# Optimization experiments

Hardware: AMD Instinct MI355X
Metric: run time of the kernel (lower is better)

The kernel has to match this reference:

```python
import jax, jax.numpy as jnp
import numpy as np

N_HEADS = 16
NEG_BIG = float(-2**32 + 1)  # value the original writes into masked positions


def setup_inputs() -> dict:
    key = jax.random.key(0)
    ks = jax.random.split(key, 5)
    B, T, D = 64, 256, 1024
    s = 1.0 / np.sqrt(D)
    return {
        "x": jax.random.normal(ks[0], (B, T, D), jnp.float32),
        "pos_emb": jax.random.normal(ks[1], (T, D), jnp.float32),
        "Wq": jax.random.normal(ks[2], (D, D), jnp.float32) * s,
        "Wk": jax.random.normal(ks[3], (D, D), jnp.float32) * s,
        "Wv": jax.random.normal(ks[4], (D, D), jnp.float32) * s,
    }


def reference(x, pos_emb, Wq, Wk, Wv):
    B, T, D = x.shape
    H = N_HEADS
    dh = D // H
    # add position embeddings (same arange positions for every batch row)
    temporal = x + pos_emb[None, :T, :]            # [B, T, D]
    q = temporal @ Wq                              # [B, T, D]
    k = temporal @ Wk
    v = temporal @ Wv
    # chunk along feature dim into H heads, concatenate along batch dim -> [H*B, T, dh]
    def split_heads(t):
        return jnp.concatenate(jnp.split(t, H, axis=2), axis=0)
    q_, k_, v_ = split_heads(q), split_heads(k), split_heads(v)
    scores = jnp.einsum('btd,bsd->bts', q_, k_) / jnp.sqrt(jnp.asarray(T, x.dtype))  # [H*B, T, T]
    # original masks the LOWER triangle (tril > 0 -> padding), faithful to source
    tril = jnp.tril(jnp.ones((T, T), x.dtype))
    scores = jnp.where(tril > 0, jnp.asarray(NEG_BIG, x.dtype), scores)
    # original applies softmax over dim=0 (the batch*head axis), faithful to source
    probs = jax.nn.softmax(scores, axis=0)         # [H*B, T, T]
    out = jnp.einsum('bts,bsd->btd', probs, v_)    # [H*B, T, dh]
    # merge heads back: chunk along batch dim, concatenate along feature dim
    out = jnp.concatenate(jnp.split(out, H, axis=0), axis=-1)  # [B, T, D]
    return out
```

## Files before the change

### kernel.cpp

```cpp
#include <hip/hip_runtime.h>

constexpr int SEQ = 256;
constexpr int DIM = 1024;
constexpr float SCALE = 0.0625f;

typedef __attribute__((ext_vector_type(8))) short bf16x8;
typedef __attribute__((ext_vector_type(4))) float f32x4;
typedef unsigned short ushort_t;
typedef unsigned int uint_t;

__device__ __forceinline__ void gld_lds16(const void* g, void* l) {
  __builtin_amdgcn_global_load_lds(
      (const __attribute__((address_space(1))) unsigned int*)g,
      (__attribute__((address_space(3))) unsigned int*)l, 16, 0, 0);
}

__device__ __forceinline__ ushort_t f2bf(float f) {
  uint_t u = __float_as_uint(f);
  return (ushort_t)((u + 0x7fffu + ((u >> 16) & 1u)) >> 16);
}

__global__ __launch_bounds__(256)
void prep_a(const float* __restrict__ x, const float* __restrict__ pos,
            ushort_t* __restrict__ Ab) {
  const size_t idx = ((size_t)blockIdx.x * 256 + threadIdx.x) * 8;
  const int m = (int)(idx >> 10), k = (int)(idx & 1023);
  float4 x0 = *(const float4*)(x + idx);
  float4 x1 = *(const float4*)(x + idx + 4);
  const float* pp = pos + ((size_t)(m & 255) << 10) + k;
  float4 p0 = *(const float4*)pp;
  float4 p1 = *(const float4*)(pp + 4);
  uint_t w0 = (uint_t)f2bf(x0.x + p0.x) | ((uint_t)f2bf(x0.y + p0.y) << 16);
  uint_t w1 = (uint_t)f2bf(x0.z + p0.z) | ((uint_t)f2bf(x0.w + p0.w) << 16);
  uint_t w2 = (uint_t)f2bf(x1.x + p1.x) | ((uint_t)f2bf(x1.y + p1.y) << 16);
  uint_t w3 = (uint_t)f2bf(x1.z + p1.z) | ((uint_t)f2bf(x1.w + p1.w) << 16);
  *(uint4*)&Ab[idx] = make_uint4(w0, w1, w2, w3);
}

__global__ __launch_bounds__(256)
void pack_w(const float* __restrict__ Wq, const float* __restrict__ Wk,
            const float* __restrict__ Wv, ushort_t* __restrict__ Bp) {
  const float* W = (blockIdx.z == 0) ? Wq : (blockIdx.z == 1) ? Wk : Wv;
  const int n  = blockIdx.x * 256 + threadIdx.x;
  const int k8 = blockIdx.y * 8;
  uint_t h[8];
#pragma unroll
  for (int i = 0; i < 8; ++i) h[i] = f2bf(W[(size_t)(k8 + i) * DIM + n]);
  uint_t hp[4];
#pragma unroll
  for (int j = 0; j < 4; ++j) hp[j] = h[2 * j] | (h[2 * j + 1] << 16);
  const int np = blockIdx.z * 1024 + n;
  const int nb = np >> 8, nl = np & 255;
  const int kc = k8 >> 6, kk = k8 & 63;
  size_t base = (((size_t)nb * 16 + kc) * 256 + nl) * 64 + kk;
  *(uint4*)&Bp[base] = make_uint4(hp[0], hp[1], hp[2], hp[3]);
}

__global__ __launch_bounds__(512, 2)
void qkv_mfma(const ushort_t* __restrict__ Ab, const ushort_t* __restrict__ Bp,
              ushort_t* __restrict__ q_bf, ushort_t* __restrict__ k_bf,
              ushort_t* __restrict__ vT_bf) {
  const int nb = blockIdx.x;
  const int mb = blockIdx.y;
  const int tid = (int)threadIdx.x;
  const int wave = tid >> 6, lane = tid & 63;
  const int wm = wave >> 2, wn = wave & 3;
  const int l15 = lane & 15, quad = lane >> 4;

  __shared__ ushort_t smem[65536];

  const int r8 = lane >> 3;
  const int lc8 = ((lane & 7) ^ r8) * 8;
  const size_t a_row = ((size_t)(mb * 256 + wave * 8 + r8)) << 10;
  const size_t b_row = ((size_t)((nb * 16) * 256 + wave * 8 + r8)) << 6;
  const int wb = wave * 512;

#define SA(q, tt, c) gld_lds16(Ab + a_row + ((size_t)(q) << 16) + (size_t)(tt) * 64 + lc8, \
                               smem + (c) * 32768 + (q) * 4096 + wb)
#define SB(q, tt, c) gld_lds16(Bp + b_row + (size_t)(tt) * 16384 + (q) * 4096 + lc8, \
                               smem + (c) * 32768 + 16384 + (q) * 4096 + wb)

  const int swz = l15 & 7;
  const int cko0 = (quad ^ swz) * 8;
  const int cko1 = ((4 + quad) ^ swz) * 8;
  const int arow0 = (wm * 128 + l15) * 64;
  const int brow0 = (wn * 64 + l15) * 64;

  f32x4 acc[8][4] = {};
  bf16x8 af[4][2], bf[4][2];

#define LDA_II(IH, ii) do { \
    const int ro = arow0 + ((IH) * 64 + (ii) * 16) * 64; \
    af[ii][0] = *(const bf16x8*)&Ac[ro + cko0]; \
    af[ii][1] = *(const bf16x8*)&Ac[ro + cko1]; } while (0)
#define LDB_J(J) do { const int ro = brow0 + (J) * 1024; \
    bf[J][0] = *(const bf16x8*)&Bc[ro + cko0]; \
    bf[J][1] = *(const bf16x8*)&Bc[ro + cko1]; } while (0)
#define MMQ(IH, II0, II1, J0) do { \
    _Pragma("unroll") for (int ks = 0; ks < 2; ++ks) \
    _Pragma("unroll") for (int ii = (II0); ii < (II1); ++ii) \
    _Pragma("unroll") for (int jj = 0; jj < 2; ++jj) \
      acc[(IH) * 4 + ii][(J0) + jj] = __builtin_amdgcn_mfma_f32_16x16x32_bf16( \
          af[ii][ks], bf[(J0) + jj][ks], acc[(IH) * 4 + ii][(J0) + jj], 0, 0, 0); \
    } while (0)

  SA(0, 0, 0); SA(2, 0, 0); SB(0, 0, 0); SB(1, 0, 0); SB(2, 0, 0); SB(3, 0, 0);
  SA(1, 0, 0); SA(3, 0, 0);
  SB(0, 1, 1); SB(1, 1, 1); SA(0, 1, 1); SA(2, 1, 1);
  asm volatile("s_waitcnt vmcnt(6)" ::: "memory");
  __builtin_amdgcn_s_barrier();

  for (int t = 0; t < 16; ++t) {
    const int cur = t & 1, nxt = cur ^ 1;
    const int tn  = (t < 15) ? t + 1 : 15;
    const int tn2 = (t < 14) ? t + 2 : 15;
    const ushort_t* Ac = &smem[cur * 32768];
    const ushort_t* Bc = Ac + 16384;
    LDA_II(0, 0); LDA_II(0, 1); LDA_II(0, 2); LDA_II(0, 3);
    LDB_J(0); LDB_J(1);
    SB(2, tn, nxt); SB(3, tn, nxt);
    __builtin_amdgcn_s_barrier();
    LDB_J(2); LDB_J(3);
    SA(1, tn, nxt); SA(3, tn, nxt);
    asm volatile("s_waitcnt lgkmcnt(4)" ::: "memory");
    __builtin_amdgcn_s_setprio(1);
    MMQ(0, 0, 4, 0);
    __builtin_amdgcn_s_setprio(0);
    asm volatile("s_waitcnt vmcnt(8)" ::: "memory");
    __builtin_amdgcn_s_barrier();
    asm volatile("s_waitcnt lgkmcnt(0)" ::: "memory");
    __builtin_amdgcn_s_setprio(1);
    MMQ(0, 0, 2, 2);
    __builtin_amdgcn_s_setprio(0);
    LDA_II(1, 0); LDA_II(1, 1);
    __builtin_amdgcn_s_setprio(1);
    MMQ(0, 2, 4, 2);
    __builtin_amdgcn_s_setprio(0);
    LDA_II(1, 2); LDA_II(1, 3);
    __builtin_amdgcn_s_barrier();
    SB(0, tn2, cur); SB(1, tn2, cur);
    asm volatile("s_waitcnt lgkmcnt(0)" ::: "memory");
    __builtin_amdgcn_s_setprio(1);
    MMQ(1, 0, 4, 2);
    __builtin_amdgcn_s_setprio(0);
    __builtin_amdgcn_s_barrier();
    SA(0, tn2, cur); SA(2, tn2, cur);
    __builtin_amdgcn_s_setprio(1);
    MMQ(1, 0, 4, 0);
    __builtin_amdgcn_s_setprio(0);
    asm volatile("s_waitcnt vmcnt(6)" ::: "memory");
    __builtin_amdgcn_s_barrier();
  }

  asm volatile("s_waitcnt vmcnt(0)" ::: "memory");
  const int wq = nb >> 2;
  const int h  = (nb & 3) * 4 + wn;
  if (wq < 2) {
    ushort_t* base = ((wq == 0) ? q_bf : k_bf) + (size_t)(mb * 16 + h) * (SEQ * 64);
    const int tb = wm * 128 + quad * 4;
#pragma unroll
    for (int i = 0; i < 8; ++i)
#pragma unroll
      for (int j = 0; j < 4; ++j) {
        const int d = j * 16 + l15;
#pragma unroll
        for (int r = 0; r < 4; ++r)
          base[(size_t)(tb + i * 16 + r) * 64 + d] = f2bf(acc[i][j][r]);
      }
  } else {
    __builtin_amdgcn_s_barrier();
    ushort_t* L = &smem[wave * 4608];
    ushort_t* vbase = vT_bf + (size_t)(mb * 16 + h) * (64 * SEQ) + wm * 128;
    const int tc = (lane & 7) * 8;
#pragma unroll
    for (int g = 0; g < 2; ++g) {
#pragma unroll
      for (int ii = 0; ii < 4; ++ii)
#pragma unroll
        for (int j = 0; j < 4; ++j) {
          f32x4 v = acc[g * 4 + ii][j];
          uint_t lo = (uint_t)f2bf(v[0]) | ((uint_t)f2bf(v[1]) << 16);
          uint_t hi = (uint_t)f2bf(v[2]) | ((uint_t)f2bf(v[3]) << 16);
          *(uint2*)&L[(j * 16 + l15) * 72 + ii * 16 + quad * 4] = make_uint2(lo, hi);
        }
#pragma unroll
      for (int u = 0; u < 8; ++u) {
        const int d = u * 8 + r8;
        uint4 val = *(const uint4*)&L[d * 72 + tc];
        *(uint4*)&vbase[(size_t)d * SEQ + g * 64 + tc] = val;
      }
    }
  }
#undef SA
#undef SB
#undef LDA_II
#undef LDB_J
#undef MMQ
}

__global__ __launch_bounds__(256)
void stats_mfma(const ushort_t* __restrict__ qb, const ushort_t* __restrict__ kb,
                float* __restrict__ part_l) {
  const int p = blockIdx.x, g = blockIdx.y;
  int tt, ss;
  if (p < 4) { tt = p; ss = p; }
  else {
    const int idx = p - 4;
    tt = (idx < 3) ? 0 : (idx < 5) ? 1 : 2;
    ss = (idx < 3) ? idx + 1 : (idx < 5) ? idx - 1 : 3;
  }
  const bool diag = (p < 4);
  const int tid = threadIdx.x, wave = tid >> 6, lane = tid & 63;
  const int l15 = lane & 15, quad = lane >> 4;

  __shared__ __attribute__((aligned(16))) float red[4][64 * 68];

  f32x4 lacc[4][4] = {};

  for (int i4 = 0; i4 < 4; ++i4) {
    const int bp = g * 16 + wave * 4 + i4;
    const int bh = (bp & 63) * 16 + (bp >> 6);
    const ushort_t* qt = qb + (size_t)bh * (SEQ * 64) + (size_t)(tt * 64) * 64;
    const ushort_t* kt = kb + (size_t)bh * (SEQ * 64) + (size_t)(ss * 64) * 64;
    bf16x8 aq[4][2], bk[4][2];
#pragma unroll
    for (int m = 0; m < 4; ++m)
#pragma unroll
      for (int ks = 0; ks < 2; ++ks) {
        aq[m][ks] = *(const bf16x8*)&qt[(m * 16 + l15) * 64 + ks * 32 + quad * 8];
        bk[m][ks] = *(const bf16x8*)&kt[(m * 16 + l15) * 64 + ks * 32 + quad * 8];
      }
    f32x4 sf[4][4] = {};
#pragma unroll
    for (int ks = 0; ks < 2; ++ks)
#pragma unroll
      for (int m = 0; m < 4; ++m)
#pragma unroll
        for (int n = 0; n < 4; ++n)
          sf[m][n] = __builtin_amdgcn_mfma_f32_16x16x32_bf16(aq[m][ks], bk[n][ks], sf[m][n], 0, 0, 0);
#pragma unroll
    for (int m = 0; m < 4; ++m)
#pragma unroll
      for (int n = 0; n < 4; ++n)
#pragma unroll
        for (int r = 0; r < 4; ++r) {
          float e = __expf(sf[m][n][r] * SCALE);
          if (diag) {
            const int t = tt * 64 + m * 16 + quad * 4 + r;
            const int s = ss * 64 + n * 16 + l15;
            e = (s > t) ? e : 1.0f;
          }
          lacc[m][n][r] += e;
        }
  }
  float* R = red[wave];
#pragma unroll
  for (int m = 0; m < 4; ++m)
#pragma unroll
    for (int r = 0; r < 4; ++r) {
      const int row = m * 16 + quad * 4 + r;
#pragma unroll
      for (int n = 0; n < 4; ++n)
        R[row * 68 + n * 16 + l15] = lacc[m][n][r];
    }
  __syncthreads();
  const int trow = tid >> 2, c0 = (tid & 3) * 16;
  const float* r0 = &red[0][trow * 68 + c0];
  const float* r1 = &red[1][trow * 68 + c0];
  const float* r2 = &red[2][trow * 68 + c0];
  const float* r3 = &red[3][trow * 68 + c0];
  float* pl = part_l + (size_t)g * (SEQ * SEQ) + (size_t)(tt * 64 + trow) * SEQ + ss * 64 + c0;
#pragma unroll
  for (int c = 0; c < 16; c += 4) {
    float4 s0 = *(const float4*)&r0[c];
    float4 s1 = *(const float4*)&r1[c];
    float4 s2 = *(const float4*)&r2[c];
    float4 s3 = *(const float4*)&r3[c];
    float4 o;
    o.x = (s0.x + s1.x) + (s2.x + s3.x);
    o.y = (s0.y + s1.y) + (s2.y + s3.y);
    o.z = (s0.z + s1.z) + (s2.z + s3.z);
    o.w = (s0.w + s1.w) + (s2.w + s3.w);
    *(float4*)&pl[c] = o;
  }
}

__global__ __launch_bounds__(256)
void merge_kernel(const float* __restrict__ part_l, float* __restrict__ inv_lT) {
  const int i = blockIdx.x * 256 + threadIdx.x;
  const int t = i >> 8, s = i & 255;
  float invv;
  if (s <= t) invv = 1.0f / 1024.0f;
  else {
    const float* p = part_l + i;
    float a0 = 0.f, a1 = 0.f, a2 = 0.f, a3 = 0.f,
          a4 = 0.f, a5 = 0.f, a6 = 0.f, a7 = 0.f;
    for (int g = 0; g < 64; g += 8) {
      const float* q = p + ((size_t)g << 16);
      a0 += q[0ull << 16]; a1 += q[1ull << 16]; a2 += q[2ull << 16]; a3 += q[3ull << 16];
      a4 += q[4ull << 16]; a5 += q[5ull << 16]; a6 += q[6ull << 16]; a7 += q[7ull << 16];
    }
    invv = 1.0f / (((a0 + a1) + (a2 + a3)) + ((a4 + a5) + (a6 + a7)));
  }
  inv_lT[s * SEQ + t] = invv;
}

__global__ __launch_bounds__(256)
void pv_mfma(const ushort_t* __restrict__ qb, const ushort_t* __restrict__ kb,
             const ushort_t* __restrict__ vtb, const float* __restrict__ inv_lT,
             float* __restrict__ out) {
  const int bh = blockIdx.x;
  const int b = bh >> 4, h = bh & 15;
  const int tid = threadIdx.x, wave = tid >> 6, lane = tid & 63;
  const int l15 = lane & 15, quad = lane >> 4;
  const int t0 = wave * 64;

  __shared__ ushort_t Plds[4][64][72];
  ushort_t (*Pw)[72] = Plds[wave];

  const ushort_t* qq = qb + (size_t)bh * (SEQ * 64);
  const ushort_t* kk = kb + (size_t)bh * (SEQ * 64);
  const ushort_t* vv = vtb + (size_t)bh * (64 * SEQ);

  bf16x8 qf[4][2];
#pragma unroll
  for (int nt = 0; nt < 4; ++nt)
#pragma unroll
    for (int ks = 0; ks < 2; ++ks)
      qf[nt][ks] = *(const bf16x8*)&qq[(t0 + nt * 16 + l15) * 64 + ks * 32 + quad * 8];

  f32x4 o[4][4] = {};

  for (int sc = 0; sc < 4; ++sc) {
    if (sc < wave) {
      const uint_t c = 0x3A803A80u;
      const uint4 cc = make_uint4(c, c, c, c);
#pragma unroll
      for (int u = 0; u < 8; ++u) *(uint4*)&Pw[lane][u * 8] = cc;
    } else {
      bf16x8 kf[4][2];
#pragma unroll
      for (int ms = 0; ms < 4; ++ms)
#pragma unroll
        for (int ks = 0; ks < 2; ++ks)
          kf[ms][ks] = *(const bf16x8*)&kk[(sc * 64 + ms * 16 + l15) * 64 + ks * 32 + quad * 8];
      f32x4 sf[4][4] = {};
#pragma unroll
      for (int ks = 0; ks < 2; ++ks)
#pragma unroll
        for (int ms = 0; ms < 4; ++ms)
#pragma unroll
          for (int nt = 0; nt < 4; ++nt)
            sf[ms][nt] = __builtin_amdgcn_mfma_f32_16x16x32_bf16(kf[ms][ks], qf[nt][ks], sf[ms][nt], 0, 0, 0);
      const bool dg = (sc == wave);
      const int t = t0 + l15;
#pragma unroll
      for (int ms = 0; ms < 4; ++ms)
#pragma unroll
        for (int nt = 0; nt < 4; ++nt) {
          const int sb = sc * 64 + ms * 16 + quad * 4;
          const int tc = t + nt * 16;
          ushort_t pb[4];
#pragma unroll
          for (int r = 0; r < 4; ++r) {
            const int s = sb + r;
            float e = __expf(sf[ms][nt][r] * SCALE);
            if (dg) e = (s > tc) ? e : 1.0f;
            pb[r] = f2bf(e * inv_lT[(size_t)s * SEQ + tc]);
          }
          uint_t lo = (uint_t)pb[0] | ((uint_t)pb[1] << 16);
          uint_t hi = (uint_t)pb[2] | ((uint_t)pb[3] << 16);
          *(uint2*)&Pw[nt * 16 + l15][ms * 16 + quad * 4] = make_uint2(lo, hi);
        }
    }
    bf16x8 vf[4][2], pf[4][2];
#pragma unroll
    for (int nd = 0; nd < 4; ++nd)
#pragma unroll
      for (int ks = 0; ks < 2; ++ks)
        vf[nd][ks] = *(const bf16x8*)&vv[(nd * 16 + l15) * SEQ + sc * 64 + ks * 32 + quad * 8];
#pragma unroll
    for (int mt = 0; mt < 4; ++mt)
#pragma unroll
      for (int ks = 0; ks < 2; ++ks)
        pf[mt][ks] = *(const bf16x8*)&Pw[mt * 16 + l15][ks * 32 + quad * 8];
#pragma unroll
    for (int ks = 0; ks < 2; ++ks)
#pragma unroll
      for (int mt = 0; mt < 4; ++mt)
#pragma unroll
        for (int nd = 0; nd < 4; ++nd)
          o[mt][nd] = __builtin_amdgcn_mfma_f32_16x16x32_bf16(pf[mt][ks], vf[nd][ks], o[mt][nd], 0, 0, 0);
  }

  float* ob = out + (size_t)b * SEQ * DIM + h * 64;
#pragma unroll
  for (int mt = 0; mt < 4; ++mt)
#pragma unroll
    for (int r = 0; r < 4; ++r) {
      const int t = t0 + mt * 16 + quad * 4 + r;
#pragma unroll
      for (int nd = 0; nd < 4; ++nd)
        ob[(size_t)t * DIM + nd * 16 + l15] = o[mt][nd][r];
    }
}

extern "C" void kernel_launch(void* const* d_in, const int* in_sizes, int n_in,
                              void* d_out, int out_size, void* d_ws, size_t ws_size,
                              hipStream_t stream) {
  const float* x   = (const float*)d_in[0];
  const float* pos = (const float*)d_in[1];
  const float* Wq  = (const float*)d_in[2];
  const float* Wk  = (const float*)d_in[3];
  const float* Wv  = (const float*)d_in[4];
  float* out = (float*)d_out;

  ushort_t* Ab = (ushort_t*)d_out;
  ushort_t* Bp = (ushort_t*)((char*)d_out + 33554432);

  char* W = (char*)d_ws;
  ushort_t* q_bf   = (ushort_t*)(W);
  ushort_t* k_bf   = (ushort_t*)(W + 33554432);
  ushort_t* vT_bf  = (ushort_t*)(W + 67108864);
  float*    part_l = (float*)  (W + 100663296);
  float*    inv_lT = (float*)  (W + 167772160);

  prep_a<<<dim3(8192), 256, 0, stream>>>(x, pos, Ab);
  pack_w<<<dim3(4, 128, 3), 256, 0, stream>>>(Wq, Wk, Wv, Bp);
  qkv_mfma<<<dim3(12, 64), 512, 0, stream>>>(Ab, Bp, q_bf, k_bf, vT_bf);
  stats_mfma<<<dim3(10, 64), 256, 0, stream>>>(q_bf, k_bf, part_l);
  merge_kernel<<<dim3(SEQ * SEQ / 256), 256, 0, stream>>>(part_l, inv_lT);
  pv_mfma<<<dim3(1024), 256, 0, stream>>>(q_bf, k_bf, vT_bf, inv_lT, out);
}
```

Baseline: 350.7 us.

## Retile QKV GEMM to 128x256 tiles with triple-buffered K=32 pipeline

The QKV projection GEMM moves from 256x256 output tiles with a double-buffered K=64 schedule to 128x256 tiles with a three-stage K=32 ring buffer. Shared memory shrinks and launch bounds allow four blocks per CU, and the grid doubles along M. The aim is more occupancy and more blocks to hide memory latency. In exchange, per-block data reuse drops and barriers per unit of work rise.

```diff
diff --git a/kernel.cpp b/kernel.cpp
--- a/kernel.cpp
+++ b/kernel.cpp
@@ -56,7 +56,7 @@
   *(uint4*)&Bp[base] = make_uint4(hp[0], hp[1], hp[2], hp[3]);
 }
 
-__global__ __launch_bounds__(512, 2)
+__global__ __launch_bounds__(512, 4)
 void qkv_mfma(const ushort_t* __restrict__ Ab, const ushort_t* __restrict__ Bp,
               ushort_t* __restrict__ q_bf, ushort_t* __restrict__ k_bf,
               ushort_t* __restrict__ vT_bf) {
@@ -64,138 +64,122 @@
   const int mb = blockIdx.y;
   const int tid = (int)threadIdx.x;
   const int wave = tid >> 6, lane = tid & 63;
-  const int wm = wave >> 2, wn = wave & 3;
+  const int wr = wave >> 2, wc = wave & 3;
   const int l15 = lane & 15, quad = lane >> 4;
 
-  __shared__ ushort_t smem[65536];
-
-  const int r8 = lane >> 3;
-  const int lc8 = ((lane & 7) ^ r8) * 8;
-  const size_t a_row = ((size_t)(mb * 256 + wave * 8 + r8)) << 10;
-  const size_t b_row = ((size_t)((nb * 16) * 256 + wave * 8 + r8)) << 6;
-  const int wb = wave * 512;
-
-#define SA(q, tt, c) gld_lds16(Ab + a_row + ((size_t)(q) << 16) + (size_t)(tt) * 64 + lc8, \
-                               smem + (c) * 32768 + (q) * 4096 + wb)
-#define SB(q, tt, c) gld_lds16(Bp + b_row + (size_t)(tt) * 16384 + (q) * 4096 + lc8, \
-                               smem + (c) * 32768 + 16384 + (q) * 4096 + wb)
-
-  const int swz = l15 & 7;
-  const int cko0 = (quad ^ swz) * 8;
-  const int cko1 = ((4 + quad) ^ swz) * 8;
-  const int arow0 = (wm * 128 + l15) * 64;
-  const int brow0 = (wn * 64 + l15) * 64;
-
-  f32x4 acc[8][4] = {};
-  bf16x8 af[4][2], bf[4][2];
-
-#define LDA_II(IH, ii) do { \
-    const int ro = arow0 + ((IH) * 64 + (ii) * 16) * 64; \
-    af[ii][0] = *(const bf16x8*)&Ac[ro + cko0]; \
-    af[ii][1] = *(const bf16x8*)&Ac[ro + cko1]; } while (0)
-#define LDB_J(J) do { const int ro = brow0 + (J) * 1024; \
-    bf[J][0] = *(const bf16x8*)&Bc[ro + cko0]; \
-    bf[J][1] = *(const bf16x8*)&Bc[ro + cko1]; } while (0)
-#define MMQ(IH, II0, II1, J0) do { \
-    _Pragma("unroll") for (int ks = 0; ks < 2; ++ks) \
-    _Pragma("unroll") for (int ii = (II0); ii < (II1); ++ii) \
-    _Pragma("unroll") for (int jj = 0; jj < 2; ++jj) \
-      acc[(IH) * 4 + ii][(J0) + jj] = __builtin_amdgcn_mfma_f32_16x16x32_bf16( \
-          af[ii][ks], bf[(J0) + jj][ks], acc[(IH) * 4 + ii][(J0) + jj], 0, 0, 0); \
-    } while (0)
-
-  SA(0, 0, 0); SA(2, 0, 0); SB(0, 0, 0); SB(1, 0, 0); SB(2, 0, 0); SB(3, 0, 0);
-  SA(1, 0, 0); SA(3, 0, 0);
-  SB(0, 1, 1); SB(1, 1, 1); SA(0, 1, 1); SA(2, 1, 1);
+  __shared__ ushort_t smem[36864];
+
+  const int ar = tid >> 2, ap = tid & 3;
+  const int al = ap ^ ((ar >> 1) & 3);
+  const ushort_t* a_src = Ab + ((size_t)(mb * 128 + ar) << 10) + al * 8;
+  const ushort_t* b_src0 = Bp + ((size_t)(nb * 16) * 256 + ar) * 64 + al * 8;
+  const ushort_t* b_src1 = b_src0 + 128 * 64;
+
+#define STAGE(T, R3) do { \
+    const size_t ka = (size_t)(T) * 32; \
+    const size_t kb = (size_t)((T) >> 1) * 16384 + (size_t)((T) & 1) * 32; \
+    gld_lds16(a_src + ka, smem + (R3) * 4096 + wave * 512); \
+    gld_lds16(b_src0 + kb, smem + 12288 + (R3) * 8192 + wave * 512); \
+    gld_lds16(b_src1 + kb, smem + 12288 + (R3) * 8192 + 4096 + wave * 512); \
+  } while (0)
+
+  int aofs[4], bofs[4];
+#pragma unroll
+  for (int m = 0; m < 4; ++m) {
+    const int row = wr * 64 + m * 16 + l15;
+    aofs[m] = row * 64 + ((quad ^ ((row >> 1) & 3)) * 16);
+  }
+#pragma unroll
+  for (int j = 0; j < 4; ++j) {
+    const int n = wc * 64 + j * 16 + l15;
+    bofs[j] = n * 64 + ((quad ^ ((n >> 1) & 3)) * 16);
+  }
+
+  f32x4 acc[4][4] = {};
+  bf16x8 af[4], bfr[4];
+
+#define READS(R3) do { \
+    const char* ab_ = (const char*)smem + (R3) * 8192; \
+    const char* bb_ = (const char*)smem + 24576 + (R3) * 16384; \
+    _Pragma("unroll") for (int m = 0; m < 4; ++m) af[m] = *(const bf16x8*)(ab_ + aofs[m]); \
+    _Pragma("unroll") for (int j = 0; j < 4; ++j) bfr[j] = *(const bf16x8*)(bb_ + bofs[j]); \
+  } while (0)
+#define MFMA16() do { \
+    __builtin_amdgcn_s_setprio(1); \
+    _Pragma("unroll") for (int m = 0; m < 4; ++m) \
+    _Pragma("unroll") for (int j = 0; j < 4; ++j) \
+      acc[m][j] = __builtin_amdgcn_mfma_f32_16x16x32_bf16(af[m], bfr[j], acc[m][j], 0, 0, 0); \
+    __builtin_amdgcn_s_setprio(0); } while (0)
+
+  STAGE(0, 0); STAGE(1, 1); STAGE(2, 2);
   asm volatile("s_waitcnt vmcnt(6)" ::: "memory");
+
+  int r3 = 0;
+  for (int t = 0; t < 29; ++t) {
+    __builtin_amdgcn_s_barrier();
+    READS(r3);
+    asm volatile("s_waitcnt lgkmcnt(0)" ::: "memory");
+    __builtin_amdgcn_s_barrier();
+    STAGE(t + 3, r3);
+    MFMA16();
+    asm volatile("s_waitcnt vmcnt(6)" ::: "memory");
+    r3 = (r3 == 2) ? 0 : r3 + 1;
+  }
   __builtin_amdgcn_s_barrier();
-
-  for (int t = 0; t < 16; ++t) {
-    const int cur = t & 1, nxt = cur ^ 1;
-    const int tn  = (t < 15) ? t + 1 : 15;
-    const int tn2 = (t < 14) ? t + 2 : 15;
-    const ushort_t* Ac = &smem[cur * 32768];
-    const ushort_t* Bc = Ac + 16384;
-    LDA_II(0, 0); LDA_II(0, 1); LDA_II(0, 2); LDA_II(0, 3);
-    LDB_J(0); LDB_J(1);
-    SB(2, tn, nxt); SB(3, tn, nxt);
-    __builtin_amdgcn_s_barrier();
-    LDB_J(2); LDB_J(3);
-    SA(1, tn, nxt); SA(3, tn, nxt);
-    asm volatile("s_waitcnt lgkmcnt(4)" ::: "memory");
-    __builtin_amdgcn_s_setprio(1);
-    MMQ(0, 0, 4, 0);
-    __builtin_amdgcn_s_setprio(0);
-    asm volatile("s_waitcnt vmcnt(8)" ::: "memory");
-    __builtin_amdgcn_s_barrier();
-    asm volatile("s_waitcnt lgkmcnt(0)" ::: "memory");
-    __builtin_amdgcn_s_setprio(1);
-    MMQ(0, 0, 2, 2);
-    __builtin_amdgcn_s_setprio(0);
-    LDA_II(1, 0); LDA_II(1, 1);
-    __builtin_amdgcn_s_setprio(1);
-    MMQ(0, 2, 4, 2);
-    __builtin_amdgcn_s_setprio(0);
-    LDA_II(1, 2); LDA_II(1, 3);
-    __builtin_amdgcn_s_barrier();
-    SB(0, tn2, cur); SB(1, tn2, cur);
-    asm volatile("s_waitcnt lgkmcnt(0)" ::: "memory");
-    __builtin_amdgcn_s_setprio(1);
-    MMQ(1, 0, 4, 2);
-    __builtin_amdgcn_s_setprio(0);
-    __builtin_amdgcn_s_barrier();
-    SA(0, tn2, cur); SA(2, tn2, cur);
-    __builtin_amdgcn_s_setprio(1);
-    MMQ(1, 0, 4, 0);
-    __builtin_amdgcn_s_setprio(0);
-    asm volatile("s_waitcnt vmcnt(6)" ::: "memory");
-    __builtin_amdgcn_s_barrier();
-  }
-
+  READS(2);
+  asm volatile("s_waitcnt lgkmcnt(0)" ::: "memory");
+  __builtin_amdgcn_s_barrier();
+  MFMA16();
+  asm volatile("s_waitcnt vmcnt(3)" ::: "memory");
+  __builtin_amdgcn_s_barrier();
+  READS(0);
+  asm volatile("s_waitcnt lgkmcnt(0)" ::: "memory");
+  __builtin_amdgcn_s_barrier();
+  MFMA16();
   asm volatile("s_waitcnt vmcnt(0)" ::: "memory");
+  __builtin_amdgcn_s_barrier();
+  READS(1);
+  asm volatile("s_waitcnt lgkmcnt(0)" ::: "memory");
+  MFMA16();
+
   const int wq = nb >> 2;
-  const int h  = (nb & 3) * 4 + wn;
+  const int h  = (nb & 3) * 4 + wc;
+  const int b  = mb >> 1;
+  const int trow0 = (mb & 1) * 128 + wr * 64;
   if (wq < 2) {
-    ushort_t* base = ((wq == 0) ? q_bf : k_bf) + (size_t)(mb * 16 + h) * (SEQ * 64);
-    const int tb = wm * 128 + quad * 4;
-#pragma unroll
-    for (int i = 0; i < 8; ++i)
+    ushort_t* base = ((wq == 0) ? q_bf : k_bf) + (size_t)(b * 16 + h) * (SEQ * 64);
+#pragma unroll
+    for (int m = 0; m < 4; ++m)
 #pragma unroll
       for (int j = 0; j < 4; ++j) {
         const int d = j * 16 + l15;
 #pragma unroll
         for (int r = 0; r < 4; ++r)
-          base[(size_t)(tb + i * 16 + r) * 64 + d] = f2bf(acc[i][j][r]);
+          base[(size_t)(trow0 + m * 16 + quad * 4 + r) * 64 + d] = f2bf(acc[m][j][r]);
       }
   } else {
     __builtin_amdgcn_s_barrier();
-    ushort_t* L = &smem[wave * 4608];
-    ushort_t* vbase = vT_bf + (size_t)(mb * 16 + h) * (64 * SEQ) + wm * 128;
-    const int tc = (lane & 7) * 8;
-#pragma unroll
-    for (int g = 0; g < 2; ++g) {
-#pragma unroll
-      for (int ii = 0; ii < 4; ++ii)
-#pragma unroll
-        for (int j = 0; j < 4; ++j) {
-          f32x4 v = acc[g * 4 + ii][j];
-          uint_t lo = (uint_t)f2bf(v[0]) | ((uint_t)f2bf(v[1]) << 16);
-          uint_t hi = (uint_t)f2bf(v[2]) | ((uint_t)f2bf(v[3]) << 16);
-          *(uint2*)&L[(j * 16 + l15) * 72 + ii * 16 + quad * 4] = make_uint2(lo, hi);
-        }
-#pragma unroll
-      for (int u = 0; u < 8; ++u) {
-        const int d = u * 8 + r8;
-        uint4 val = *(const uint4*)&L[d * 72 + tc];
-        *(uint4*)&vbase[(size_t)d * SEQ + g * 64 + tc] = val;
+    ushort_t* L = smem + wave * 4608;
+#pragma unroll
+    for (int m = 0; m < 4; ++m)
+#pragma unroll
+      for (int j = 0; j < 4; ++j) {
+        uint_t lo = (uint_t)f2bf(acc[m][j][0]) | ((uint_t)f2bf(acc[m][j][1]) << 16);
+        uint_t hi = (uint_t)f2bf(acc[m][j][2]) | ((uint_t)f2bf(acc[m][j][3]) << 16);
+        *(uint2*)&L[(j * 16 + l15) * 72 + m * 16 + quad * 4] = make_uint2(lo, hi);
       }
+    ushort_t* vbase = vT_bf + (size_t)(b * 16 + h) * (64 * SEQ) + trow0;
+    const int dr = lane >> 3, tc = (lane & 7) * 8;
+#pragma unroll
+    for (int u = 0; u < 8; ++u) {
+      const int d = u * 8 + dr;
+      uint4 val = *(const uint4*)&L[d * 72 + tc];
+      *(uint4*)&vbase[(size_t)d * SEQ + tc] = val;
     }
   }
-#undef SA
-#undef SB
-#undef LDA_II
-#undef LDB_J
-#undef MMQ
+#undef STAGE
+#undef READS
+#undef MFMA16
 }
 
 __global__ __launch_bounds__(256)
@@ -427,7 +411,7 @@
 
   prep_a<<<dim3(8192), 256, 0, stream>>>(x, pos, Ab);
   pack_w<<<dim3(4, 128, 3), 256, 0, stream>>>(Wq, Wk, Wv, Bp);
-  qkv_mfma<<<dim3(12, 64), 512, 0, stream>>>(Ab, Bp, q_bf, k_bf, vT_bf);
+  qkv_mfma<<<dim3(12, 128), 512, 0, stream>>>(Ab, Bp, q_bf, k_bf, vT_bf);
   stats_mfma<<<dim3(10, 64), 256, 0, stream>>>(q_bf, k_bf, part_l);
   merge_kernel<<<dim3(SEQ * SEQ / 256), 256, 0, stream>>>(part_l, inv_lT);
   pv_mfma<<<dim3(1024), 256, 0, stream>>>(q_bf, k_bf, vT_bf, inv_lT, out);
```

Result: no change. 353.5 us (+0.8%).
